# Kernel optimization log

Hardware: AMD Instinct MI355X
Metric: run time of the kernel (lower is better)

The kernel has to match this reference:

```python
import jax, jax.numpy as jnp
import numpy as np
from jax import lax


def _h0_entropy(img):
    """Persistence entropy of the 0-dim sublevel-set persistence diagram of a 2D
    image, using the vertex-based cubical complex (pixels = vertices, 4-neighbor
    edges with filtration value max(endpoints)). Essential (infinite) class is
    excluded. Computed via Kruskal-style union-find with the elder rule."""
    H, W = img.shape
    N = H * W
    vals = img.reshape(N)
    vals_sg = lax.stop_gradient(vals)  # pairing indices are non-differentiable

    idx = jnp.arange(N, dtype=jnp.int32).reshape(H, W)
    eu = jnp.concatenate([idx[:, :-1].ravel(), idx[:-1, :].ravel()])
    ev = jnp.concatenate([idx[:, 1:].ravel(), idx[1:, :].ravel()])
    E = eu.shape[0]  # H*(W-1) + (H-1)*W

    # process edges in increasing filtration order (sublevel filtration)
    w_sg = jnp.maximum(vals_sg[eu], vals_sg[ev])
    order = jnp.argsort(w_sg)
    eu = eu[order]
    ev = ev[order]

    def find(parent, u):
        return lax.while_loop(lambda x: parent[x] != x, lambda x: parent[x], u)

    def body(i, st):
        parent, rb, ob, odu, odv = st
        u = eu[i]
        v = ev[i]
        ru = find(parent, u)
        rv = find(parent, v)
        # one-shot path compression
        parent = parent.at[u].set(ru).at[v].set(rv)
        bu = rb[ru]  # birth-vertex index of each root's component
        bv = rb[rv]
        u_young = vals_sg[bu] >= vals_sg[bv]  # elder rule: later birth dies
        younger = jnp.where(u_young, ru, rv)
        elder = jnp.where(u_young, rv, ru)
        diff = ru != rv
        ob = ob.at[i].set(jnp.where(diff, rb[younger], -1))
        odu = odu.at[i].set(jnp.where(diff, u, 0))
        odv = odv.at[i].set(jnp.where(diff, v, 0))
        parent = parent.at[younger].set(jnp.where(diff, elder, younger))
        return (parent, rb, ob, odu, odv)

    init = (
        jnp.arange(N, dtype=jnp.int32),          # parent
        jnp.arange(N, dtype=jnp.int32),          # birth vertex per root
        -jnp.ones(E, dtype=jnp.int32),           # birth vertex per pair
        jnp.zeros(E, dtype=jnp.int32),           # death edge endpoint u
        jnp.zeros(E, dtype=jnp.int32),           # death edge endpoint v
    )
    _, _, ob, odu, odv = lax.fori_loop(0, E, body, init)

    valid = ob >= 0
    births = vals[jnp.clip(ob, 0)]
    deaths = jnp.maximum(vals[odu], vals[odv])
    pers = jnp.where(valid, deaths - births, 0.0)
    pers = jnp.maximum(pers, 0.0)
    total = jnp.sum(pers)
    p = pers / jnp.maximum(total, jnp.asarray(1e-12, pers.dtype))
    safe_p = jnp.where(p > 0, p, 1.0)
    return -jnp.sum(jnp.where(p > 0, p * jnp.log(safe_p), 0.0))


def setup_inputs() -> dict:
    key = jax.random.key(0)
    x = jax.random.normal(key, (8, 8, 96, 96), dtype=jnp.float32)
    return {"x": x}


def reference(x):
    B, C, H, W = x.shape
    flat = x.reshape(B * C, H, W)
    ents = jax.vmap(_h0_entropy)(flat)  # [B*C]
    # TopoHead stacks per-channel features along dim=1; maxdim=0 -> one
    # persistence-entropy value per (batch, channel).
    return ents.reshape(B, C, 1)
```

## Files before the change

kernel.cpp:

```cpp
#include <hip/hip_runtime.h>

#define H_ 96
#define W_ 96
#define NV (H_ * W_)
#define NT 1024
#define WELEM 576
#define NSUB 9

#define ARENA_BYTES 126976

__device__ __forceinline__ float keyToFloat(unsigned int k) {
  return __uint_as_float((k & 0x80000000u) ? (k ^ 0x80000000u) : ~k);
}
__device__ __forceinline__ unsigned int bitsToKey(unsigned int b) {
  return b ^ ((b & 0x80000000u) ? 0xFFFFFFFFu : 0x80000000u);
}

__global__ __launch_bounds__(NT, 1)
void topo_pk(const float* __restrict__ x, float* __restrict__ out) {
  __shared__ unsigned int arenaW[ARENA_BYTES / 4];
  __shared__ unsigned int waveS[16];
  __shared__ unsigned int waveB[16];
  __shared__ double Td[16], Sd[16];
  unsigned char* arena = (unsigned char*)arenaW;
  unsigned int*   Ka    = (unsigned int*)(arena);
  unsigned int*   Kb    = (unsigned int*)(arena + 36864);
  unsigned short* Pa    = (unsigned short*)(arena + 73728);
  unsigned short* Pb    = (unsigned short*)(arena + 92160);
  unsigned int*   hist  = (unsigned int*)(arena + 110592);
  unsigned short* parU  = (unsigned short*)(arena + 92160);
  unsigned int*   claim = (unsigned int*)(arena + 36864);

  const int tid = threadIdx.x;
  const int wv = tid >> 6, ln = tid & 63;
  const float* img = x + (size_t)blockIdx.x * NV;

  for (int i = tid; i < NV; i += NT) {
    Ka[i] = bitsToKey(__float_as_uint(img[i]));
    Pa[i] = (unsigned short)i;
  }
  __syncthreads();

  const int wbase = wv * WELEM;
  for (int pass = 0; pass < 4; ++pass) {
    const unsigned int*   Ks = (pass & 1) ? Kb : Ka;
    const unsigned short* Ps = (pass & 1) ? Pb : Pa;
    unsigned int*   Kd = (pass & 1) ? Ka : Kb;
    unsigned short* Pd = (pass & 1) ? Pa : Pb;
    const int sh = pass << 3;

    for (int i = tid; i < 16 * 256; i += NT) hist[i] = 0u;
    __syncthreads();

    unsigned kreg[NSUB];
    unsigned rk[NSUB];
    #pragma unroll
    for (int j = 0; j < NSUB; ++j) {
      const unsigned k = Ks[wbase + j * 64 + ln];
      kreg[j] = k;
      const unsigned d = (k >> sh) & 255u;
      unsigned long long mask = ~0ull;
      #pragma unroll
      for (int b = 0; b < 8; ++b) {
        const unsigned long long bb = __ballot((d >> b) & 1u);
        mask &= ((d >> b) & 1u) ? bb : ~bb;
      }
      const unsigned long long below = mask & ((1ull << ln) - 1ull);
      const unsigned old = hist[wv * 256 + d];
      rk[j] = (d << 16) | (old + (unsigned)__popcll(below));
      if (below == 0ull)
        hist[wv * 256 + d] = old + (unsigned)__popcll(mask);
    }
    __syncthreads();

    {
      unsigned v0, v1, v2, v3;
      const int s0 = tid * 4;
      v0 = hist[((s0 + 0) & 15) * 256 + ((s0 + 0) >> 4)];
      v1 = hist[((s0 + 1) & 15) * 256 + ((s0 + 1) >> 4)];
      v2 = hist[((s0 + 2) & 15) * 256 + ((s0 + 2) >> 4)];
      v3 = hist[((s0 + 3) & 15) * 256 + ((s0 + 3) >> 4)];
      const unsigned ts = v0 + v1 + v2 + v3;
      unsigned incl = ts;
      #pragma unroll
      for (int off = 1; off < 64; off <<= 1) {
        const unsigned n = (unsigned)__shfl_up((int)incl, off, 64);
        if (ln >= off) incl += n;
      }
      if (ln == 63) waveS[wv] = incl;
      __syncthreads();
      if (tid < 16) {
        unsigned s = 0;
        for (int q = 0; q < 16; ++q) { if (q == tid) break; s += waveS[q]; }
        waveB[tid] = s;
      }
      __syncthreads();
      unsigned run = waveB[wv] + (incl - ts);
      hist[((s0 + 0) & 15) * 256 + ((s0 + 0) >> 4)] = run; run += v0;
      hist[((s0 + 1) & 15) * 256 + ((s0 + 1) >> 4)] = run; run += v1;
      hist[((s0 + 2) & 15) * 256 + ((s0 + 2) >> 4)] = run; run += v2;
      hist[((s0 + 3) & 15) * 256 + ((s0 + 3) >> 4)] = run;
    }
    __syncthreads();

    #pragma unroll
    for (int j = 0; j < NSUB; ++j) {
      const int e = wbase + j * 64 + ln;
      const unsigned d = rk[j] >> 16;
      const unsigned dest = hist[wv * 256 + d] + (rk[j] & 0xFFFFu);
      Kd[dest] = kreg[j];
      Pd[dest] = Ps[e];
    }
    __syncthreads();
  }

  for (int t = tid; t < NV; t += NT) parU[Pa[t]] = (unsigned short)(0x8000u | (unsigned)t);
  for (int i = tid; i < NV; i += NT) claim[i] = 0xFFFFFFFFu;
  __syncthreads();

  double T = 0.0, S = 0.0;
  for (int ch = 0; ch < NV / NT; ++ch) {
    const int t = ch * NT + tid;
    const int vid = (int)Pa[t];
    const unsigned keyT = Ka[t];
    const float vt = keyToFloat(keyT);
    const int r = vid / W_, c = vid - r * W_;
    const int nv0 = vid - 1, nv1 = vid + 1, nv2 = vid - W_, nv3 = vid + W_;
    const bool bb0 = (c > 0), bb1 = (c < W_ - 1), bb2 = (r > 0), bb3 = (r < H_ - 1);
    const unsigned kk0 = bb0 ? bitsToKey(__float_as_uint(img[nv0])) : 0xFFFFFFFFu;
    const unsigned kk1 = bb1 ? bitsToKey(__float_as_uint(img[nv1])) : 0xFFFFFFFFu;
    const unsigned kk2 = bb2 ? bitsToKey(__float_as_uint(img[nv2])) : 0xFFFFFFFFu;
    const unsigned kk3 = bb3 ? bitsToKey(__float_as_uint(img[nv3])) : 0xFFFFFFFFu;
    const bool inc0 = bb0 && (kk0 <= keyT);
    const bool inc1 = bb1 && (kk1 <= keyT);
    const bool inc2 = bb2 && (kk2 <= keyT);
    const bool inc3 = bb3 && (kk3 <= keyT);
    int x0 = inc0 ? nv0 : vid, x1 = inc1 ? nv1 : vid;
    int x2 = inc2 ? nv2 : vid, x3 = inc3 ? nv3 : vid;
    unsigned e0 = 0, e1 = 0, e2 = 0, e3 = 0;
    bool committed = false;

    for (;;) {
      if (!committed) {
        bool d0 = !inc0, d1 = !inc1, d2 = !inc2, d3 = !inc3;
        while (!(d0 && d1 && d2 && d3)) {
          if (!d0) { unsigned e = parU[x0]; if (e & 0x8000u) { e0 = e; d0 = true; } else x0 = (int)e; }
          if (!d1) { unsigned e = parU[x1]; if (e & 0x8000u) { e1 = e; d1 = true; } else x1 = (int)e; }
          if (!d2) { unsigned e = parU[x2]; if (e & 0x8000u) { e2 = e; d2 = true; } else x2 = (int)e; }
          if (!d3) { unsigned e = parU[x3]; if (e & 0x8000u) { e3 = e; d3 = true; } else x3 = (int)e; }
        }
        if (inc0 && nv0 != x0) parU[nv0] = (unsigned short)x0;
        if (inc1 && nv1 != x1) parU[nv1] = (unsigned short)x1;
        if (inc2 && nv2 != x2) parU[nv2] = (unsigned short)x2;
        if (inc3 && nv3 != x3) parU[nv3] = (unsigned short)x3;
      }
      bool u0 = false, u1 = false, u2 = false, u3 = false, uv = false;
      int mvid = vid;
      int rr0 = 0, rr1 = 0, rr2 = 0, rr3 = 0;
      if (!committed) {
        int mrank = t;
        rr0 = (int)(e0 & 0x3FFFu); rr1 = (int)(e1 & 0x3FFFu);
        rr2 = (int)(e2 & 0x3FFFu); rr3 = (int)(e3 & 0x3FFFu);
        if (inc0 && rr0 < mrank) { mrank = rr0; mvid = x0; }
        if (inc1 && rr1 < mrank) { mrank = rr1; mvid = x1; }
        if (inc2 && rr2 < mrank) { mrank = rr2; mvid = x2; }
        if (inc3 && rr3 < mrank) { mrank = rr3; mvid = x3; }
        u0 = inc0 && (x0 != mvid);
        u1 = inc1 && (x1 != mvid) && !(inc0 && x1 == x0);
        u2 = inc2 && (x2 != mvid) && !(inc0 && x2 == x0) && !(inc1 && x2 == x1);
        u3 = inc3 && (x3 != mvid) && !(inc0 && x3 == x0) && !(inc1 && x3 == x1) && !(inc2 && x3 == x2);
        uv = (mvid != vid);
        if (u0) atomicMin(&claim[x0], (unsigned)tid);
        if (u1) atomicMin(&claim[x1], (unsigned)tid);
        if (u2) atomicMin(&claim[x2], (unsigned)tid);
        if (u3) atomicMin(&claim[x3], (unsigned)tid);
        if (uv) atomicMin(&claim[vid], (unsigned)tid);
      }
      __syncthreads();
      bool win = !committed;
      if (!committed) {
        if (u0 && claim[x0] != (unsigned)tid) win = false;
        if (u1 && claim[x1] != (unsigned)tid) win = false;
        if (u2 && claim[x2] != (unsigned)tid) win = false;
        if (u3 && claim[x3] != (unsigned)tid) win = false;
        if (uv && claim[vid] != (unsigned)tid) win = false;
      }
      __syncthreads();
      if (win && !committed) {
        if (u0) { const float p = vt - keyToFloat(Ka[rr0]);
                  if (p > 0.0f) { T += (double)p; S += (double)(p * logf(p)); }
                  parU[x0] = (unsigned short)mvid; }
        if (u1) { const float p = vt - keyToFloat(Ka[rr1]);
                  if (p > 0.0f) { T += (double)p; S += (double)(p * logf(p)); }
                  parU[x1] = (unsigned short)mvid; }
        if (u2) { const float p = vt - keyToFloat(Ka[rr2]);
                  if (p > 0.0f) { T += (double)p; S += (double)(p * logf(p)); }
                  parU[x2] = (unsigned short)mvid; }
        if (u3) { const float p = vt - keyToFloat(Ka[rr3]);
                  if (p > 0.0f) { T += (double)p; S += (double)(p * logf(p)); }
                  parU[x3] = (unsigned short)mvid; }
        if (uv) parU[vid] = (unsigned short)mvid;
        committed = true;
      }
      if (u0) claim[x0] = 0xFFFFFFFFu;
      if (u1) claim[x1] = 0xFFFFFFFFu;
      if (u2) claim[x2] = 0xFFFFFFFFu;
      if (u3) claim[x3] = 0xFFFFFFFFu;
      if (uv) claim[vid] = 0xFFFFFFFFu;
      if (__syncthreads_count(!committed ? 1 : 0) == 0) break;
    }
  }

  #pragma unroll
  for (int off = 32; off > 0; off >>= 1) {
    T += __shfl_down(T, off, 64);
    S += __shfl_down(S, off, 64);
  }
  if (ln == 0) { Td[wv] = T; Sd[wv] = S; }
  __syncthreads();
  if (tid == 0) {
    double Tt = 0.0, St = 0.0;
    for (int q = 0; q < 16; ++q) { Tt += Td[q]; St += Sd[q]; }
    out[blockIdx.x] = (Tt > 0.0) ? (float)(log(Tt) - St / Tt) : 0.0f;
  }
}

extern "C" void kernel_launch(void* const* d_in, const int* in_sizes, int n_in,
                              void* d_out, int out_size, void* d_ws, size_t ws_size,
                              hipStream_t stream) {
  (void)n_in; (void)out_size; (void)d_ws; (void)ws_size;
  const float* x = (const float*)d_in[0];
  float* out = (float*)d_out;
  int n_img = in_sizes[0] / NV;
  if (n_img <= 0) n_img = 1;
  topo_pk<<<n_img, NT, 0, stream>>>(x, out);
}
```

Measured before the change: 154.9 us.

## Fuse image load into first radix pass and drop claim-reset barrier via round-tagged claims

The first radix pass now reads keys straight from global memory and uses element indices as payload, which removes the separate initial copy loop and its barrier. The claim protocol in the union phase now uses round-decreasing claim values, so claims no longer need resetting each round. That drops one __syncthreads and the reset stores per round. The counter allows about a million rounds before wrapping, and correctness depends on later rounds always producing smaller values than stale claims.

```diff
diff --git a/kernel.cpp b/kernel.cpp
--- a/kernel.cpp
+++ b/kernel.cpp
@@ -35,12 +35,6 @@
   const int wv = tid >> 6, ln = tid & 63;
   const float* img = x + (size_t)blockIdx.x * NV;
 
-  for (int i = tid; i < NV; i += NT) {
-    Ka[i] = bitsToKey(__float_as_uint(img[i]));
-    Pa[i] = (unsigned short)i;
-  }
-  __syncthreads();
-
   const int wbase = wv * WELEM;
   for (int pass = 0; pass < 4; ++pass) {
     const unsigned int*   Ks = (pass & 1) ? Kb : Ka;
@@ -56,7 +50,8 @@
     unsigned rk[NSUB];
     #pragma unroll
     for (int j = 0; j < NSUB; ++j) {
-      const unsigned k = Ks[wbase + j * 64 + ln];
+      const int e = wbase + j * 64 + ln;
+      const unsigned k = (pass == 0) ? bitsToKey(__float_as_uint(img[e])) : Ks[e];
       kreg[j] = k;
       const unsigned d = (k >> sh) & 255u;
       unsigned long long mask = ~0ull;
@@ -109,7 +104,7 @@
       const unsigned d = rk[j] >> 16;
       const unsigned dest = hist[wv * 256 + d] + (rk[j] & 0xFFFFu);
       Kd[dest] = kreg[j];
-      Pd[dest] = Ps[e];
+      Pd[dest] = (pass == 0) ? (unsigned short)e : Ps[e];
     }
     __syncthreads();
   }
@@ -119,6 +114,7 @@
   __syncthreads();
 
   double T = 0.0, S = 0.0;
+  unsigned gr = 0;
   for (int ch = 0; ch < NV / NT; ++ch) {
     const int t = ch * NT + tid;
     const int vid = (int)Pa[t];
@@ -141,6 +137,8 @@
     bool committed = false;
 
     for (;;) {
+      const unsigned cval = ((0x000FFFFFu - gr) << 10) | (unsigned)tid;
+      ++gr;
       if (!committed) {
         bool d0 = !inc0, d1 = !inc1, d2 = !inc2, d3 = !inc3;
         while (!(d0 && d1 && d2 && d3)) {
@@ -170,43 +168,37 @@
         u2 = inc2 && (x2 != mvid) && !(inc0 && x2 == x0) && !(inc1 && x2 == x1);
         u3 = inc3 && (x3 != mvid) && !(inc0 && x3 == x0) && !(inc1 && x3 == x1) && !(inc2 && x3 == x2);
         uv = (mvid != vid);
-        if (u0) atomicMin(&claim[x0], (unsigned)tid);
-        if (u1) atomicMin(&claim[x1], (unsigned)tid);
-        if (u2) atomicMin(&claim[x2], (unsigned)tid);
-        if (u3) atomicMin(&claim[x3], (unsigned)tid);
-        if (uv) atomicMin(&claim[vid], (unsigned)tid);
+        if (u0) atomicMin(&claim[x0], cval);
+        if (u1) atomicMin(&claim[x1], cval);
+        if (u2) atomicMin(&claim[x2], cval);
+        if (u3) atomicMin(&claim[x3], cval);
+        if (uv) atomicMin(&claim[vid], cval);
       }
       __syncthreads();
-      bool win = !committed;
       if (!committed) {
-        if (u0 && claim[x0] != (unsigned)tid) win = false;
-        if (u1 && claim[x1] != (unsigned)tid) win = false;
-        if (u2 && claim[x2] != (unsigned)tid) win = false;
-        if (u3 && claim[x3] != (unsigned)tid) win = false;
-        if (uv && claim[vid] != (unsigned)tid) win = false;
-      }
-      __syncthreads();
-      if (win && !committed) {
-        if (u0) { const float p = vt - keyToFloat(Ka[rr0]);
-                  if (p > 0.0f) { T += (double)p; S += (double)(p * logf(p)); }
-                  parU[x0] = (unsigned short)mvid; }
-        if (u1) { const float p = vt - keyToFloat(Ka[rr1]);
-                  if (p > 0.0f) { T += (double)p; S += (double)(p * logf(p)); }
-                  parU[x1] = (unsigned short)mvid; }
-        if (u2) { const float p = vt - keyToFloat(Ka[rr2]);
-                  if (p > 0.0f) { T += (double)p; S += (double)(p * logf(p)); }
-                  parU[x2] = (unsigned short)mvid; }
-        if (u3) { const float p = vt - keyToFloat(Ka[rr3]);
-                  if (p > 0.0f) { T += (double)p; S += (double)(p * logf(p)); }
-                  parU[x3] = (unsigned short)mvid; }
-        if (uv) parU[vid] = (unsigned short)mvid;
-        committed = true;
-      }
-      if (u0) claim[x0] = 0xFFFFFFFFu;
-      if (u1) claim[x1] = 0xFFFFFFFFu;
-      if (u2) claim[x2] = 0xFFFFFFFFu;
-      if (u3) claim[x3] = 0xFFFFFFFFu;
-      if (uv) claim[vid] = 0xFFFFFFFFu;
+        bool win = true;
+        if (u0 && claim[x0] != cval) win = false;
+        if (u1 && claim[x1] != cval) win = false;
+        if (u2 && claim[x2] != cval) win = false;
+        if (u3 && claim[x3] != cval) win = false;
+        if (uv && claim[vid] != cval) win = false;
+        if (win) {
+          if (u0) { const float p = vt - keyToFloat(Ka[rr0]);
+                    if (p > 0.0f) { T += (double)p; S += (double)(p * logf(p)); }
+                    parU[x0] = (unsigned short)mvid; }
+          if (u1) { const float p = vt - keyToFloat(Ka[rr1]);
+                    if (p > 0.0f) { T += (double)p; S += (double)(p * logf(p)); }
+                    parU[x1] = (unsigned short)mvid; }
+          if (u2) { const float p = vt - keyToFloat(Ka[rr2]);
+                    if (p > 0.0f) { T += (double)p; S += (double)(p * logf(p)); }
+                    parU[x2] = (unsigned short)mvid; }
+          if (u3) { const float p = vt - keyToFloat(Ka[rr3]);
+                    if (p > 0.0f) { T += (double)p; S += (double)(p * logf(p)); }
+                    parU[x3] = (unsigned short)mvid; }
+          if (uv) parU[vid] = (unsigned short)mvid;
+          committed = true;
+        }
+      }
       if (__syncthreads_count(!committed ? 1 : 0) == 0) break;
     }
   }
```

Measured after the change: 148.7 us. 1.04x faster.
